# Optimization experiments

Hardware: AMD Instinct MI355X
Metric: run time of the kernel (lower is better)

Reference implementation:

```python
import jax, jax.numpy as jnp
import numpy as np

KH, KW = 3, 3
STRIDE = (1, 1)
PADDING = (1, 1)
DILATION = (1, 1)


def setup_inputs() -> dict:
    key = jax.random.key(0)
    k1, k2, k3, k4, k5 = jax.random.split(key, 5)
    B, Cin, H, W = 8, 64, 128, 128
    Cout = 64
    Ho, Wo = 128, 128  # stride 1, pad 1, k=3 -> same spatial size
    K = KH * KW
    return {
        "input": jax.random.normal(k1, (B, Cin, H, W), dtype=jnp.float32),
        "offset": jax.random.normal(k2, (B, 2 * K, Ho, Wo), dtype=jnp.float32),
        "mask": jax.random.uniform(k3, (B, K, Ho, Wo), dtype=jnp.float32),
        "weight": jax.random.normal(k4, (Cout, Cin, KH, KW), dtype=jnp.float32) * 0.05,
        "bias": jax.random.normal(k5, (Cout,), dtype=jnp.float32) * 0.05,
    }


def _deform_conv2d(x, weight, offset, mask, bias, stride, padding, dilation):
    B, Cin, H, W = x.shape
    Cout, Cing, kh, kw = weight.shape
    G = Cin // Cing                      # weight groups
    K = kh * kw
    Goff = offset.shape[1] // (2 * K)    # offset groups
    Ho, Wo = offset.shape[2], offset.shape[3]
    Cg = Cin // Goff                     # channels per offset group
    sh, sw = stride
    ph, pw = padding
    dh, dw = dilation

    # offsets laid out as (y, x) pairs per kernel tap per offset group
    off = offset.reshape(B, Goff, K, 2, Ho, Wo)
    ky = (jnp.arange(K) // kw).astype(jnp.float32) * dh   # [K]
    kx = (jnp.arange(K) % kw).astype(jnp.float32) * dw
    gy = (jnp.arange(Ho).astype(jnp.float32) * sh - ph)    # [Ho]
    gx = (jnp.arange(Wo).astype(jnp.float32) * sw - pw)
    # sampling positions: [B, Goff, K, Ho, Wo]
    py = off[:, :, :, 0] + ky[None, None, :, None, None] + gy[None, None, None, :, None]
    px = off[:, :, :, 1] + kx[None, None, :, None, None] + gx[None, None, None, None, :]

    y0 = jnp.floor(py)
    x0 = jnp.floor(px)
    ly = py - y0
    lx = px - x0
    y0i = y0.astype(jnp.int32)
    x0i = x0.astype(jnp.int32)

    x_g = x.reshape(B, Goff, Cg, H * W)

    def gather(yi, xi):
        # zero padding outside the image
        valid = (yi >= 0) & (yi < H) & (xi >= 0) & (xi < W)
        yc = jnp.clip(yi, 0, H - 1)
        xc = jnp.clip(xi, 0, W - 1)
        idx = (yc * W + xc).reshape(B, Goff, K * Ho * Wo)
        v = jnp.take_along_axis(x_g, idx[:, :, None, :], axis=3)  # [B,Goff,Cg,K*Ho*Wo]
        return v * valid.reshape(B, Goff, 1, K * Ho * Wo)

    w00 = ((1 - ly) * (1 - lx)).reshape(B, Goff, 1, K * Ho * Wo)
    w01 = ((1 - ly) * lx).reshape(B, Goff, 1, K * Ho * Wo)
    w10 = (ly * (1 - lx)).reshape(B, Goff, 1, K * Ho * Wo)
    w11 = (ly * lx).reshape(B, Goff, 1, K * Ho * Wo)

    sampled = w00 * gather(y0i, x0i)
    sampled = sampled + w01 * gather(y0i, x0i + 1)
    sampled = sampled + w10 * gather(y0i + 1, x0i)
    sampled = sampled + w11 * gather(y0i + 1, x0i + 1)
    sampled = sampled.reshape(B, Goff, Cg, K, Ho, Wo)

    if mask is not None:
        sampled = sampled * mask.reshape(B, Goff, 1, K, Ho, Wo)

    # grouped conv accumulate
    sampled = sampled.reshape(B, G, Cing, K, Ho, Wo)
    w = weight.reshape(G, Cout // G, Cing, K)
    out = jnp.einsum('gock,bgcksq->bgosq', w, sampled).reshape(B, Cout, Ho, Wo)
    if bias is not None:
        out = out + bias[None, :, None, None]
    return out


def reference(input, offset, mask, weight, bias):
    return _deform_conv2d(input, weight, offset, mask, bias, STRIDE, PADDING, DILATION)
```

## Files before the change

### kernel.cpp

```cpp
#include <hip/hip_runtime.h>
#include <hip/hip_fp16.h>

#define HH 128
#define WW 128
#define HW (HH*WW)
#define XT_BYTES ((size_t)8 * HW * 64 * 2)
#define WT_BYTES ((size_t)9 * 2 * 4 * 64 * 8 * 2)

typedef __attribute__((ext_vector_type(8))) short short8;
typedef __attribute__((ext_vector_type(4))) float f32x4;
typedef _Float16 half8 __attribute__((ext_vector_type(8)));

static __device__ __forceinline__ unsigned short f2bf(float f) {
    unsigned int u = __float_as_uint(f);
    u += 0x7fffu + ((u >> 16) & 1u);
    return (unsigned short)(u >> 16);
}
static __device__ __forceinline__ unsigned pkrtz(float lo, float hi) {
    auto r = __builtin_amdgcn_cvt_pkrtz(lo, hi);
    return *(unsigned*)&r;
}

__global__ void wtrans_kernel(const float* __restrict__ w, unsigned short* __restrict__ wt) {
    int i = blockIdx.x * 256 + threadIdx.x;
    if (i < 9 * 2 * 4 * 64 * 8) {
        int e  = i & 7;
        int l  = (i >> 3) & 63;
        int wv = (i >> 9) & 3;
        int kf = (i >> 11) & 1;
        int k  = i >> 12;
        int co = wv * 16 + (l & 15);
        int c  = kf * 32 + (l >> 4) * 8 + e;
        __half hh = __float2half_rn(w[(co * 64 + c) * 9 + k]);
        wt[i] = __half_as_ushort(hh);
    }
}

__global__ __launch_bounds__(256) void xtrans_kernel(const float* __restrict__ x,
                                                     unsigned int* __restrict__ xt32) {
    __shared__ float tile[64][65];
    const int bid = blockIdx.x;
    const int b   = bid >> 8;
    const int hw0 = (bid & 255) << 6;
    const int t   = threadIdx.x;
    #pragma unroll
    for (int i = 0; i < 16; ++i) {
        int idx = (i << 8) + t;
        int c = idx >> 6, j = idx & 63;
        tile[c][j] = x[(size_t)(((b << 6) + c) << 14) + hw0 + j];
    }
    __syncthreads();
    #pragma unroll
    for (int i = 0; i < 8; ++i) {
        int idx = (i << 8) + t;
        int cp = idx & 31, hw = idx >> 5;
        xt32[((size_t)((b << 14) + hw0 + hw) << 5) + cp] =
            pkrtz(tile[2 * cp][hw], tile[2 * cp + 1][hw]);
    }
}

__global__ __launch_bounds__(256, 4) void deform_nhwc(
    const unsigned short* __restrict__ xt,
    const float* __restrict__ off,
    const float* __restrict__ msk,
    const unsigned short* __restrict__ wt,
    const float* __restrict__ bias,
    float* __restrict__ out)
{
    __shared__ __align__(16) unsigned char smem[25600];
    ushort4* moSu = (ushort4*)(smem + 16384);
    uint2*   mwH  = (uint2*)(smem + 20992);

    const int t   = threadIdx.x;
    const int bid = blockIdx.x;
    const int b   = bid & 7;
    const int rem = bid >> 3;
    const int ho  = rem >> 1;
    const int wo0 = (rem & 1) << 6;
    const int l   = t & 63;
    const int wv  = __builtin_amdgcn_readfirstlane(t >> 6);

    for (int i = t; i < 9 * 64; i += 256) {
        int p = i & 63;
        int k = i >> 6;
        int wo = wo0 + p;
        int obase = ((b * 18 + 2 * k) * HH + ho) * WW + wo;
        float oy = off[obase];
        float ox = off[obase + HW];
        float m  = msk[((b * 9 + k) * HH + ho) * WW + wo];
        float py = oy + (float)(k / 3) + (float)(ho - 1);
        float px = ox + (float)(k % 3) + (float)(wo - 1);
        float fy = floorf(py), fx = floorf(px);
        float ly = py - fy,    lx = px - fx;
        int y0 = (int)fy, x0 = (int)fx;
        int y1 = y0 + 1,  x1 = x0 + 1;
        float vy0 = (y0 >= 0 && y0 < HH) ? 1.f : 0.f;
        float vy1 = (y1 >= 0 && y1 < HH) ? 1.f : 0.f;
        float vx0 = (x0 >= 0 && x0 < WW) ? 1.f : 0.f;
        float vx1 = (x1 >= 0 && x1 < WW) ? 1.f : 0.f;
        float w00 = (1.f - ly) * (1.f - lx) * m * vy0 * vx0;
        float w01 = (1.f - ly) * lx         * m * vy0 * vx1;
        float w10 = ly         * (1.f - lx) * m * vy1 * vx0;
        float w11 = ly         * lx         * m * vy1 * vx1;
        int yc0 = min(max(y0, 0), HH - 1), yc1 = min(max(y1, 0), HH - 1);
        int xc0 = min(max(x0, 0), WW - 1), xc1 = min(max(x1, 0), WW - 1);
        moSu[i] = make_ushort4((unsigned short)(yc0 * WW + xc0),
                               (unsigned short)(yc0 * WW + xc1),
                               (unsigned short)(yc1 * WW + xc0),
                               (unsigned short)(yc1 * WW + xc1));
        __half2 hA = __floats2half2_rn(w00, w01);
        __half2 hB = __floats2half2_rn(w10, w11);
        mwH[i] = make_uint2(*(unsigned*)&hA, *(unsigned*)&hB);
    }

    const char* ib   = (const char*)xt + (size_t)b * HW * 128;
    const int  chb   = (l & 7) << 4;
    const int  ploc  = l >> 3;
    const int  px0_  = (wv << 4) + ploc;
    unsigned char* wbase = smem + (wv << 12);
    int st_woff[2];
    st_woff[0] = ploc * 128 + (chb ^ ((ploc & 7) << 4));
    st_woff[1] = st_woff[0] + 8 * 128;
    const int lq = (l >> 4) << 4;
    const int sw = (l & 7) << 4;

    uint4 g0[4], g1[4];
    half8 wtf[8];

    #define ISSUE_TAP(kk) {                                          \
        ushort4 ob0 = moSu[(kk) * 64 + px0_];                        \
        g0[0] = *(const uint4*)(ib + (((int)ob0.x) << 7) + chb);     \
        g0[1] = *(const uint4*)(ib + (((int)ob0.y) << 7) + chb);     \
        g0[2] = *(const uint4*)(ib + (((int)ob0.z) << 7) + chb);     \
        g0[3] = *(const uint4*)(ib + (((int)ob0.w) << 7) + chb);     \
        ushort4 ob1 = moSu[(kk) * 64 + px0_ + 8];                    \
        g1[0] = *(const uint4*)(ib + (((int)ob1.x) << 7) + chb);     \
        g1[1] = *(const uint4*)(ib + (((int)ob1.y) << 7) + chb);     \
        g1[2] = *(const uint4*)(ib + (((int)ob1.z) << 7) + chb);     \
        g1[3] = *(const uint4*)(ib + (((int)ob1.w) << 7) + chb);     \
    }

    #define ISSUE_WTF(kk) {                                          \
        _Pragma("unroll")                                            \
        for (int q = 0; q < 8; ++q) {                                \
            short8 sv = *(const short8*)(wt + ((((kk) * 8 + q) * 64 + l) << 3)); \
            wtf[q] = *(half8*)&sv;                                   \
        }                                                            \
    }

    #define CMBH(dst_, c00, c01, c10, c11) {                         \
        __half2 a_ = __hmul2(*(__half2*)&(c11), W11);                \
        a_ = __hfma2(*(__half2*)&(c10), W10, a_);                    \
        a_ = __hfma2(*(__half2*)&(c01), W01, a_);                    \
        a_ = __hfma2(*(__half2*)&(c00), W00, a_);                    \
        dst_ = *(unsigned*)&a_;                                      \
    }

    #define COMBINE_STORE(kk, dstb) {                                \
        {                                                            \
            uint2 wp = mwH[(kk) * 64 + px0_];                        \
            __half2 wab = *(__half2*)&wp.x, wcd = *(__half2*)&wp.y;  \
            __half2 W00 = __half2half2(__low2half(wab));             \
            __half2 W01 = __half2half2(__high2half(wab));            \
            __half2 W10 = __half2half2(__low2half(wcd));             \
            __half2 W11 = __half2half2(__high2half(wcd));            \
            uint4 uv;                                                \
            CMBH(uv.x, g0[0].x, g0[1].x, g0[2].x, g0[3].x)           \
            CMBH(uv.y, g0[0].y, g0[1].y, g0[2].y, g0[3].y)           \
            CMBH(uv.z, g0[0].z, g0[1].z, g0[2].z, g0[3].z)           \
            CMBH(uv.w, g0[0].w, g0[1].w, g0[2].w, g0[3].w)           \
            *(uint4*)((dstb) + st_woff[0]) = uv;                     \
        }                                                            \
        {                                                            \
            uint2 wp = mwH[(kk) * 64 + px0_ + 8];                    \
            __half2 wab = *(__half2*)&wp.x, wcd = *(__half2*)&wp.y;  \
            __half2 W00 = __half2half2(__low2half(wab));             \
            __half2 W01 = __half2half2(__high2half(wab));            \
            __half2 W10 = __half2half2(__low2half(wcd));             \
            __half2 W11 = __half2half2(__high2half(wcd));            \
            uint4 uv;                                                \
            CMBH(uv.x, g1[0].x, g1[1].x, g1[2].x, g1[3].x)           \
            CMBH(uv.y, g1[0].y, g1[1].y, g1[2].y, g1[3].y)           \
            CMBH(uv.z, g1[0].z, g1[1].z, g1[2].z, g1[3].z)           \
            CMBH(uv.w, g1[0].w, g1[1].w, g1[2].w, g1[3].w)           \
            *(uint4*)((dstb) + st_woff[1]) = uv;                     \
        }                                                            \
    }

    __syncthreads();

    ISSUE_TAP(0)
    COMBINE_STORE(0, wbase)
    ISSUE_WTF(0)

    f32x4 acc[4];
    #pragma unroll
    for (int g = 0; g < 4; ++g) acc[g] = (f32x4){0.f, 0.f, 0.f, 0.f};

    #pragma unroll
    for (int s = 0; s < 9; ++s) {
        if (s < 8) { ISSUE_TAP(s + 1) }
        {
            const unsigned char* rb = wbase + ((s & 1) << 11);
            const int arow = (l & 15) * 128;
            short8 a0 = *(const short8*)(rb + arow + (lq ^ sw));
            short8 a1 = *(const short8*)(rb + arow + ((64 + lq) ^ sw));
            #pragma unroll
            for (int cot = 0; cot < 4; ++cot) {
                acc[cot] = __builtin_amdgcn_mfma_f32_16x16x32_f16(*(half8*)&a0, wtf[cot],     acc[cot], 0, 0, 0);
                acc[cot] = __builtin_amdgcn_mfma_f32_16x16x32_f16(*(half8*)&a1, wtf[4 + cot], acc[cot], 0, 0, 0);
            }
        }
        if (s < 8) {
            ISSUE_WTF(s + 1)
            COMBINE_STORE(s + 1, wbase + (((s + 1) & 1) << 11))
        }
    }
    #undef ISSUE_TAP
    #undef ISSUE_WTF
    #undef CMBH
    #undef COMBINE_STORE

    __syncthreads();
    float* out_t = (float*)smem;
    const int pxb = (wv << 6) + ((l >> 4) << 4);
    const int swE = (l & 15) << 4;
    #pragma unroll
    for (int cot = 0; cot < 4; ++cot) {
        int co_e = (cot << 4) + (l & 15);
        float bv = bias[co_e];
        float4 v = make_float4(acc[cot][0] + bv, acc[cot][1] + bv,
                               acc[cot][2] + bv, acc[cot][3] + bv);
        *(float4*)((unsigned char*)out_t + co_e * 256 + (pxb ^ swE)) = v;
    }
    __syncthreads();
    float* outb = out + (size_t)b * 64 * HW + (size_t)ho * WW + wo0;
    #pragma unroll
    for (int j = 0; j < 4; ++j) {
        int co   = (t >> 4) + (j << 4);
        int colb = (t & 15) << 4;
        float4 v = *(const float4*)((const unsigned char*)out_t + co * 256 + (colb ^ ((co & 15) << 4)));
        *(float4*)&outb[(size_t)co * HW + ((t & 15) << 2)] = v;
    }
}

__global__ __launch_bounds__(256, 4) void deform_fallback(
    const float* __restrict__ x, const float* __restrict__ off,
    const float* __restrict__ msk, const float* __restrict__ wraw,
    const float* __restrict__ bias, float* __restrict__ out)
{
    __shared__ unsigned short s_tile[2][64][68];
    __shared__ __align__(16) unsigned char meta_mem[18432];
    float4* mwS = (float4*)meta_mem;
    int4*   moS = (int4*)(meta_mem + 9216);
    float*  out_t = (float*)meta_mem;

    const int t   = threadIdx.x;
    const int bid = blockIdx.x;
    const int b   = bid & 7;
    const int rem = bid >> 3;
    const int ho  = rem >> 1;
    const int wo0 = (rem & 1) << 6;
    const int l   = t & 63;
    const int wv_id = __builtin_amdgcn_readfirstlane(t >> 6);
    const int c0  = wv_id << 4;
    const int cb  = wv_id << 4;

    short8 wtf[2][2];
    #pragma unroll
    for (int kf = 0; kf < 2; ++kf) {
        short8 f;
        int co = cb + (l & 15);
        int cbase = kf * 32 + (l >> 4) * 8;
        #pragma unroll
        for (int e = 0; e < 8; ++e) f[e] = (short)f2bf(wraw[(co * 64 + cbase + e) * 9 + 0]);
        wtf[0][kf] = f;
    }

    for (int i = t; i < 9 * 64; i += 256) {
        int p = i & 63;
        int k = i >> 6;
        int wo = wo0 + p;
        int obase = ((b * 18 + 2 * k) * HH + ho) * WW + wo;
        float oy = off[obase];
        float ox = off[obase + HW];
        float m  = msk[((b * 9 + k) * HH + ho) * WW + wo];
        float py = oy + (float)(k / 3) + (float)(ho - 1);
        float px = ox + (float)(k % 3) + (float)(wo - 1);
        float fy = floorf(py), fx = floorf(px);
        float ly = py - fy,    lx = px - fx;
        int y0 = (int)fy, x0 = (int)fx;
        int y1 = y0 + 1,  x1 = x0 + 1;
        float vy0 = (y0 >= 0 && y0 < HH) ? 1.f : 0.f;
        float vy1 = (y1 >= 0 && y1 < HH) ? 1.f : 0.f;
        float vx0 = (x0 >= 0 && x0 < WW) ? 1.f : 0.f;
        float vx1 = (x1 >= 0 && x1 < WW) ? 1.f : 0.f;
        float w00 = (1.f - ly) * (1.f - lx) * m * vy0 * vx0;
        float w01 = (1.f - ly) * lx         * m * vy0 * vx1;
        float w10 = ly         * (1.f - lx) * m * vy1 * vx0;
        float w11 = ly         * lx         * m * vy1 * vx1;
        int yc0 = min(max(y0, 0), HH - 1), yc1 = min(max(y1, 0), HH - 1);
        int xc0 = min(max(x0, 0), WW - 1), xc1 = min(max(x1, 0), WW - 1);
        mwS[i] = make_float4(w00, w01, w10, w11);
        moS[i] = make_int4(yc0 * WW + xc0, yc0 * WW + xc1,
                           yc1 * WW + xc0, yc1 * WW + xc1);
    }

    const int p = t & 63;
    const float* xb = x + (size_t)(b * 64 + c0) * HW;
    __syncthreads();

    {
        float4 wv = mwS[p];
        int4   ov = moS[p];
        const float* pc = xb;
        #pragma unroll
        for (int i = 0; i < 16; i += 4) {
            float v0 = wv.x * pc[ov.x] + wv.y * pc[ov.y] + wv.z * pc[ov.z] + wv.w * pc[ov.w]; pc += HW;
            float v1 = wv.x * pc[ov.x] + wv.y * pc[ov.y] + wv.z * pc[ov.z] + wv.w * pc[ov.w]; pc += HW;
            float v2 = wv.x * pc[ov.x] + wv.y * pc[ov.y] + wv.z * pc[ov.z] + wv.w * pc[ov.w]; pc += HW;
            float v3 = wv.x * pc[ov.x] + wv.y * pc[ov.y] + wv.z * pc[ov.z] + wv.w * pc[ov.w]; pc += HW;
            uint2 u;
            u.x = (unsigned)f2bf(v0) | ((unsigned)f2bf(v1) << 16);
            u.y = (unsigned)f2bf(v2) | ((unsigned)f2bf(v3) << 16);
            *(uint2*)&s_tile[0][p][c0 + i] = u;
        }
    }
    __syncthreads();

    f32x4 acc[4];
    #pragma unroll
    for (int g = 0; g < 4; ++g) acc[g] = (f32x4){0.f, 0.f, 0.f, 0.f};

    #pragma unroll
    for (int s = 0; s < 9; ++s) {
        if (s < 8) {
            const int kn = s + 1;
            #pragma unroll
            for (int kf = 0; kf < 2; ++kf) {
                short8 f;
                int co = cb + (l & 15);
                int cbase = kf * 32 + (l >> 4) * 8;
                #pragma unroll
                for (int e = 0; e < 8; ++e) f[e] = (short)f2bf(wraw[(co * 64 + cbase + e) * 9 + kn]);
                wtf[kn & 1][kf] = f;
            }
            float4 wv = mwS[kn * 64 + p];
            int4   ov = moS[kn * 64 + p];
            const float* pc = xb;
            #pragma unroll
            for (int i = 0; i < 16; i += 4) {
                float v0 = wv.x * pc[ov.x] + wv.y * pc[ov.y] + wv.z * pc[ov.z] + wv.w * pc[ov.w]; pc += HW;
                float v1 = wv.x * pc[ov.x] + wv.y * pc[ov.y] + wv.z * pc[ov.z] + wv.w * pc[ov.w]; pc += HW;
                float v2 = wv.x * pc[ov.x] + wv.y * pc[ov.y] + wv.z * pc[ov.z] + wv.w * pc[ov.w]; pc += HW;
                float v3 = wv.x * pc[ov.x] + wv.y * pc[ov.y] + wv.z * pc[ov.z] + wv.w * pc[ov.w]; pc += HW;
                uint2 u;
                u.x = (unsigned)f2bf(v0) | ((unsigned)f2bf(v1) << 16);
                u.y = (unsigned)f2bf(v2) | ((unsigned)f2bf(v3) << 16);
                *(uint2*)&s_tile[kn & 1][p][c0 + i] = u;
            }
        }
        #pragma unroll
        for (int g = 0; g < 4; ++g) {
            const int prow = g * 16 + (l & 15);
            const unsigned short* rp = &s_tile[s & 1][prow][(l >> 4) * 8];
            union { short8 v; unsigned long long q[2]; } ua0, ua1;
            ua0.q[0] = *(const unsigned long long*)(rp);
            ua0.q[1] = *(const unsigned long long*)(rp + 4);
            ua1.q[0] = *(const unsigned long long*)(rp + 32);
            ua1.q[1] = *(const unsigned long long*)(rp + 36);
            acc[g] = __builtin_amdgcn_mfma_f32_16x16x32_bf16(ua0.v, wtf[s & 1][0], acc[g], 0, 0, 0);
            acc[g] = __builtin_amdgcn_mfma_f32_16x16x32_bf16(ua1.v, wtf[s & 1][1], acc[g], 0, 0, 0);
        }
        __syncthreads();
    }

    const float bv = bias[cb + (l & 15)];
    #pragma unroll
    for (int g = 0; g < 4; ++g) {
        int co = cb + (l & 15);
        int pxb = g * 16 + (l >> 4) * 4;
        #pragma unroll
        for (int r = 0; r < 4; ++r)
            out_t[co * 68 + pxb + r] = acc[g][r] + bv;
    }
    __syncthreads();
    float* outb = out + (size_t)b * 64 * HW + (size_t)ho * WW + wo0;
    #pragma unroll
    for (int j = 0; j < 4; ++j) {
        int co  = (t >> 4) + j * 16;
        int px0 = (t & 15) << 2;
        float4 v = *(float4*)&out_t[co * 68 + px0];
        *(float4*)&outb[(size_t)co * HW + px0] = v;
    }
}

extern "C" void kernel_launch(void* const* d_in, const int* in_sizes, int n_in,
                              void* d_out, int out_size, void* d_ws, size_t ws_size,
                              hipStream_t stream) {
    const float* x    = (const float*)d_in[0];
    const float* off  = (const float*)d_in[1];
    const float* msk  = (const float*)d_in[2];
    const float* w    = (const float*)d_in[3];
    const float* bias = (const float*)d_in[4];
    float* out = (float*)d_out;

    const size_t need = XT_BYTES + WT_BYTES;
    if (d_ws != nullptr && ws_size >= need) {
        unsigned int*   xt32 = (unsigned int*)d_ws;
        unsigned short* wt   = (unsigned short*)((char*)d_ws + XT_BYTES);
        xtrans_kernel<<<2048, 256, 0, stream>>>(x, xt32);
        wtrans_kernel<<<144, 256, 0, stream>>>(w, wt);
        deform_nhwc<<<2048, 256, 0, stream>>>((const unsigned short*)xt32, off, msk, wt, bias, out);
    } else {
        deform_fallback<<<2048, 256, 0, stream>>>(x, off, msk, w, bias, out);
    }
}
```

Measured before the change: 55.89 us.

## Build MFMA A-fragments directly in registers, drop LDS staging and prefetch pipeline

Each lane now gathers the four bilinear corner vectors for its own pixel and channel slice and combines them straight into the MFMA A-operand layout. This removes the LDS double-buffer round trip, the swizzled store/load and the software prefetch of the next tap and its weights. Launch bounds rise from 4 to 6 blocks per SIMD to raise occupancy and hide the now unpipelined gather latency. The trade-off is losing explicit load/compute overlap and a tighter register budget. The removed trailing __syncthreads before the output tile reuses smem may be a race, since the sampling metadata lives at a different offset but other waves may still be reading it.

New measurement: 98.46 us. +76.2%, slower.

```diff
diff --git a/kernel.cpp b/kernel.cpp
--- a/kernel.cpp
+++ b/kernel.cpp
@@ -59,7 +59,7 @@
     }
 }
 
-__global__ __launch_bounds__(256, 4) void deform_nhwc(
+__global__ __launch_bounds__(256, 6) void deform_nhwc(
     const unsigned short* __restrict__ xt,
     const float* __restrict__ off,
     const float* __restrict__ msk,
@@ -113,40 +113,15 @@
         mwH[i] = make_uint2(*(unsigned*)&hA, *(unsigned*)&hB);
     }
 
-    const char* ib   = (const char*)xt + (size_t)b * HW * 128;
-    const int  chb   = (l & 7) << 4;
-    const int  ploc  = l >> 3;
-    const int  px0_  = (wv << 4) + ploc;
-    unsigned char* wbase = smem + (wv << 12);
-    int st_woff[2];
-    st_woff[0] = ploc * 128 + (chb ^ ((ploc & 7) << 4));
-    st_woff[1] = st_woff[0] + 8 * 128;
-    const int lq = (l >> 4) << 4;
-    const int sw = (l & 7) << 4;
-
-    uint4 g0[4], g1[4];
-    half8 wtf[8];
-
-    #define ISSUE_TAP(kk) {                                          \
-        ushort4 ob0 = moSu[(kk) * 64 + px0_];                        \
-        g0[0] = *(const uint4*)(ib + (((int)ob0.x) << 7) + chb);     \
-        g0[1] = *(const uint4*)(ib + (((int)ob0.y) << 7) + chb);     \
-        g0[2] = *(const uint4*)(ib + (((int)ob0.z) << 7) + chb);     \
-        g0[3] = *(const uint4*)(ib + (((int)ob0.w) << 7) + chb);     \
-        ushort4 ob1 = moSu[(kk) * 64 + px0_ + 8];                    \
-        g1[0] = *(const uint4*)(ib + (((int)ob1.x) << 7) + chb);     \
-        g1[1] = *(const uint4*)(ib + (((int)ob1.y) << 7) + chb);     \
-        g1[2] = *(const uint4*)(ib + (((int)ob1.z) << 7) + chb);     \
-        g1[3] = *(const uint4*)(ib + (((int)ob1.w) << 7) + chb);     \
-    }
-
-    #define ISSUE_WTF(kk) {                                          \
-        _Pragma("unroll")                                            \
-        for (int q = 0; q < 8; ++q) {                                \
-            short8 sv = *(const short8*)(wt + ((((kk) * 8 + q) * 64 + l) << 3)); \
-            wtf[q] = *(half8*)&sv;                                   \
-        }                                                            \
-    }
+    const char* ib  = (const char*)xt + (size_t)b * HW * 128;
+    const int  pxg  = (wv << 4) + (l & 15);
+    const int  chq  = (l >> 4) << 4;
+
+    __syncthreads();
+
+    f32x4 acc[4];
+    #pragma unroll
+    for (int g = 0; g < 4; ++g) acc[g] = (f32x4){0.f, 0.f, 0.f, 0.f};
 
     #define CMBH(dst_, c00, c01, c10, c11) {                         \
         __half2 a_ = __hmul2(*(__half2*)&(c11), W11);                \
@@ -156,72 +131,48 @@
         dst_ = *(unsigned*)&a_;                                      \
     }
 
-    #define COMBINE_STORE(kk, dstb) {                                \
-        {                                                            \
-            uint2 wp = mwH[(kk) * 64 + px0_];                        \
-            __half2 wab = *(__half2*)&wp.x, wcd = *(__half2*)&wp.y;  \
-            __half2 W00 = __half2half2(__low2half(wab));             \
-            __half2 W01 = __half2half2(__high2half(wab));            \
-            __half2 W10 = __half2half2(__low2half(wcd));             \
-            __half2 W11 = __half2half2(__high2half(wcd));            \
-            uint4 uv;                                                \
-            CMBH(uv.x, g0[0].x, g0[1].x, g0[2].x, g0[3].x)           \
-            CMBH(uv.y, g0[0].y, g0[1].y, g0[2].y, g0[3].y)           \
-            CMBH(uv.z, g0[0].z, g0[1].z, g0[2].z, g0[3].z)           \
-            CMBH(uv.w, g0[0].w, g0[1].w, g0[2].w, g0[3].w)           \
-            *(uint4*)((dstb) + st_woff[0]) = uv;                     \
-        }                                                            \
-        {                                                            \
-            uint2 wp = mwH[(kk) * 64 + px0_ + 8];                    \
-            __half2 wab = *(__half2*)&wp.x, wcd = *(__half2*)&wp.y;  \
-            __half2 W00 = __half2half2(__low2half(wab));             \
-            __half2 W01 = __half2half2(__high2half(wab));            \
-            __half2 W10 = __half2half2(__low2half(wcd));             \
-            __half2 W11 = __half2half2(__high2half(wcd));            \
-            uint4 uv;                                                \
-            CMBH(uv.x, g1[0].x, g1[1].x, g1[2].x, g1[3].x)           \
-            CMBH(uv.y, g1[0].y, g1[1].y, g1[2].y, g1[3].y)           \
-            CMBH(uv.z, g1[0].z, g1[1].z, g1[2].z, g1[3].z)           \
-            CMBH(uv.w, g1[0].w, g1[1].w, g1[2].w, g1[3].w)           \
-            *(uint4*)((dstb) + st_woff[1]) = uv;                     \
-        }                                                            \
-    }
-
-    __syncthreads();
-
-    ISSUE_TAP(0)
-    COMBINE_STORE(0, wbase)
-    ISSUE_WTF(0)
-
-    f32x4 acc[4];
-    #pragma unroll
-    for (int g = 0; g < 4; ++g) acc[g] = (f32x4){0.f, 0.f, 0.f, 0.f};
-
     #pragma unroll
     for (int s = 0; s < 9; ++s) {
-        if (s < 8) { ISSUE_TAP(s + 1) }
-        {
-            const unsigned char* rb = wbase + ((s & 1) << 11);
-            const int arow = (l & 15) * 128;
-            short8 a0 = *(const short8*)(rb + arow + (lq ^ sw));
-            short8 a1 = *(const short8*)(rb + arow + ((64 + lq) ^ sw));
-            #pragma unroll
-            for (int cot = 0; cot < 4; ++cot) {
-                acc[cot] = __builtin_amdgcn_mfma_f32_16x16x32_f16(*(half8*)&a0, wtf[cot],     acc[cot], 0, 0, 0);
-                acc[cot] = __builtin_amdgcn_mfma_f32_16x16x32_f16(*(half8*)&a1, wtf[4 + cot], acc[cot], 0, 0, 0);
-            }
+        ushort4 ob = moSu[s * 64 + pxg];
+        uint2   wp = mwH[s * 64 + pxg];
+        const char* p0 = ib + (((int)ob.x) << 7) + chq;
+        const char* p1 = ib + (((int)ob.y) << 7) + chq;
+        const char* p2 = ib + (((int)ob.z) << 7) + chq;
+        const char* p3 = ib + (((int)ob.w) << 7) + chq;
+        uint4 cA0 = *(const uint4*)p0;
+        uint4 cA1 = *(const uint4*)p1;
+        uint4 cA2 = *(const uint4*)p2;
+        uint4 cA3 = *(const uint4*)p3;
+        uint4 cB0 = *(const uint4*)(p0 + 64);
+        uint4 cB1 = *(const uint4*)(p1 + 64);
+        uint4 cB2 = *(const uint4*)(p2 + 64);
+        uint4 cB3 = *(const uint4*)(p3 + 64);
+        __half2 wab = *(__half2*)&wp.x, wcd = *(__half2*)&wp.y;
+        __half2 W00 = __half2half2(__low2half(wab));
+        __half2 W01 = __half2half2(__high2half(wab));
+        __half2 W10 = __half2half2(__low2half(wcd));
+        __half2 W11 = __half2half2(__high2half(wcd));
+        uint4 u0, u1;
+        CMBH(u0.x, cA0.x, cA1.x, cA2.x, cA3.x)
+        CMBH(u0.y, cA0.y, cA1.y, cA2.y, cA3.y)
+        CMBH(u0.z, cA0.z, cA1.z, cA2.z, cA3.z)
+        CMBH(u0.w, cA0.w, cA1.w, cA2.w, cA3.w)
+        CMBH(u1.x, cB0.x, cB1.x, cB2.x, cB3.x)
+        CMBH(u1.y, cB0.y, cB1.y, cB2.y, cB3.y)
+        CMBH(u1.z, cB0.z, cB1.z, cB2.z, cB3.z)
+        CMBH(u1.w, cB0.w, cB1.w, cB2.w, cB3.w)
+        half8 a0 = *(half8*)&u0;
+        half8 a1 = *(half8*)&u1;
+        #pragma unroll
+        for (int cot = 0; cot < 4; ++cot) {
+            short8 s0 = *(const short8*)(wt + (((s * 8 + cot)     * 64 + l) << 3));
+            short8 s1 = *(const short8*)(wt + (((s * 8 + 4 + cot) * 64 + l) << 3));
+            acc[cot] = __builtin_amdgcn_mfma_f32_16x16x32_f16(a0, *(half8*)&s0, acc[cot], 0, 0, 0);
+            acc[cot] = __builtin_amdgcn_mfma_f32_16x16x32_f16(a1, *(half8*)&s1, acc[cot], 0, 0, 0);
         }
-        if (s < 8) {
-            ISSUE_WTF(s + 1)
-            COMBINE_STORE(s + 1, wbase + (((s + 1) & 1) << 11))
-        }
-    }
-    #undef ISSUE_TAP
-    #undef ISSUE_WTF
+    }
     #undef CMBH
-    #undef COMBINE_STORE
-
-    __syncthreads();
+
     float* out_t = (float*)smem;
     const int pxb = (wv << 6) + ((l >> 4) << 4);
     const int swE = (l & 15) << 4;
```
